# Optimization experiments

Hardware: AMD Instinct MI355X
Metric: run time of the kernel (lower is better)

## Reference

```python
import jax, jax.numpy as jnp
import numpy as np
from math import factorial

LAMBDA_MAX = 3
NU_MAX = 4
B = 200000

# --- Clebsch-Gordan coefficients (Racah formula), precomputed on host ---

def _cg_np(l1, l2, L):
    f = factorial
    C = np.zeros((2 * l1 + 1, 2 * l2 + 1, 2 * L + 1), dtype=np.float64)
    pref0 = np.sqrt((2 * L + 1) * f(L + l1 - l2) * f(L - l1 + l2) * f(l1 + l2 - L) / f(l1 + l2 + L + 1))
    for m1 in range(-l1, l1 + 1):
        for m2 in range(-l2, l2 + 1):
            M = m1 + m2
            if abs(M) > L:
                continue
            pref = pref0 * np.sqrt(f(L + M) * f(L - M) * f(l1 - m1) * f(l1 + m1) * f(l2 - m2) * f(l2 + m2))
            s = 0.0
            for k in range(0, l1 + l2 - L + 1):
                if l1 - m1 - k < 0 or l2 + m2 - k < 0 or L - l2 + m1 + k < 0 or L - l1 - m2 + k < 0:
                    continue
                s += (-1) ** k / (f(k) * f(l1 + l2 - L - k) * f(l1 - m1 - k) * f(l2 + m2 - k) * f(L - l2 + m1 + k) * f(L - l1 - m2 + k))
            C[m1 + l1, m2 + l2, M + L] = pref * s
    return C

_CG = {}

def cg(l1, l2, L):
    key = (l1, l2, L)
    if key not in _CG:
        _CG[key] = jnp.asarray(_cg_np(l1, l2, L), dtype=jnp.float32)
    return _CG[key]

# --- WignerCombiningUnrolled: CG tensor product of two equivariant kernel dicts ---

def combine(X1, X2, lam_max):
    out = {}
    for k1, K1 in X1.items():
        l1, s1 = (int(t) for t in k1.split('_'))
        for k2, K2 in X2.items():
            l2, s2 = (int(t) for t in k2.split('_'))
            for L in range(abs(l1 - l2), min(l1 + l2, lam_max) + 1):
                sig = s1 * s2 * (-1) ** (l1 + l2 + L)
                C = cg(l1, l2, L)  # [2l1+1, 2l2+1, 2L+1]
                # K_out[b,mu,mu'] = C[m1,m2,mu] C[m1',m2',mu'] K1[b,m1,m1'] K2[b,m2,m2']
                contrib = jnp.einsum('mnk,pqj,bmp,bnq->bkj', C, C, K1, K2, optimize=True)
                key = str(L) + '_' + str(sig)
                out[key] = out[key] + contrib if key in out else contrib
    return out


def setup_inputs() -> dict:
    key = jax.random.key(0)
    ks = jax.random.split(key, 4)
    return {
        'x0': jax.random.normal(ks[0], (B, 1, 1), dtype=jnp.float32),
        'x1': jax.random.normal(ks[1], (B, 3, 3), dtype=jnp.float32),
        'x2': jax.random.normal(ks[2], (B, 5, 5), dtype=jnp.float32),
        'x3': jax.random.normal(ks[3], (B, 7, 7), dtype=jnp.float32),
    }


def reference(x0, x1, x2, x3):
    # nu=1 kernels: keys 'l_1' for l = 0..lambda_max
    X = {str(l) + '_1': x for l, x in enumerate([x0, x1, x2, x3])}
    equivariant_kernels = [X]
    result = [X['0_1'][:, 0, 0, None]]
    for nu in range(2, NU_MAX + 1):
        if nu <= NU_MAX - NU_MAX // 2:
            equivariant_kernels.append(combine(equivariant_kernels[-1], equivariant_kernels[0], LAMBDA_MAX))
            result.append(equivariant_kernels[-1]['0_1'][:, 0, 0, None])
        else:
            comb = combine(
                equivariant_kernels[NU_MAX - NU_MAX // 2 - 1],
                equivariant_kernels[nu - NU_MAX + NU_MAX // 2 - 1],
                0,
            )
            result.append(comb['0_1'][:, 0, 0, None])
    return jnp.concatenate(result, axis=-1)  # [B, nu_max]
```

## Files before the change

kernel.cpp:

```cpp
#include <hip/hip_runtime.h>


#define SCHED_FENCE() __builtin_amdgcn_sched_barrier(0)

template <int N>
__device__ __forceinline__ void opaque(float (&A)[N]) {
#pragma unroll
  for (int i = 0; i < N; ++i) asm volatile("" : "+v"(A[i]));
}
__device__ __forceinline__ void opaque1(float& x) { asm volatile("" : "+v"(x)); }

constexpr double cfact(int n) { double r = 1.0; for (int i = 2; i <= n; ++i) r *= (double)i; return r; }

constexpr double csqrt(double x) {
  if (x <= 0.0) return 0.0;
  double g = x > 1.0 ? x : 1.0;
  for (int i = 0; i < 100; ++i) g = 0.5 * (g + x / g);
  return g;
}

constexpr double cg_val(int l1, int l2, int L, int m1, int m2) {
  const int M = m1 + m2;
  if (M < -L || M > L) return 0.0;
  const double pref0 = csqrt((2.0 * L + 1.0) * cfact(L + l1 - l2) * cfact(L - l1 + l2) *
                             cfact(l1 + l2 - L) / cfact(l1 + l2 + L + 1));
  const double pref = pref0 * csqrt(cfact(L + M) * cfact(L - M) * cfact(l1 - m1) *
                                    cfact(l1 + m1) * cfact(l2 - m2) * cfact(l2 + m2));
  double s = 0.0;
  for (int k = 0; k <= l1 + l2 - L; ++k) {
    if (l1 - m1 - k < 0 || l2 + m2 - k < 0 || L - l2 + m1 + k < 0 || L - l1 - m2 + k < 0) continue;
    const double t = 1.0 / (cfact(k) * cfact(l1 + l2 - L - k) * cfact(l1 - m1 - k) *
                            cfact(l2 + m2 - k) * cfact(L - l2 + m1 + k) * cfact(L - l1 - m2 + k));
    s += (k & 1) ? -t : t;
  }
  return pref * s;
}

template <int l1, int l2, int L>
struct CG2T {
  double a[2 * l1 + 1][2 * L + 1];
  constexpr CG2T() : a{} {
    for (int mi = 0; mi < 2 * l1 + 1; ++mi)
      for (int kk = 0; kk < 2 * L + 1; ++kk) {
        const int m1 = mi - l1, M = kk - L, m2 = M - m1;
        a[mi][kk] = (m2 < -l2 || m2 > l2) ? 0.0 : cg_val(l1, l2, L, m1, m2);
      }
  }
};
template <int l1, int l2, int L>
constexpr CG2T<l1, l2, L> CG2v = CG2T<l1, l2, L>();

template <int l1, int l2, int L, int W>
__device__ __forceinline__ float triElem(const float (&K1)[(2 * l1 + 1) * (2 * l1 + 1)],
                                         const float (&K2)[(2 * l2 + 1) * (2 * l2 + 1)],
                                         int kk, int jj) {
  constexpr int d1 = 2 * l1 + 1, d2 = 2 * l2 + 1;
  float a0 = 0.f, a1 = 0.f;
#pragma unroll
  for (int mi = 0; mi < d1; ++mi) {
    const int ni = (kk - L) - (mi - l1) + l2;
    if (ni < 0 || ni >= d2) continue;
#pragma unroll
    for (int pi = 0; pi < d1; ++pi) {
      const int qi = (jj - L) - (pi - l1) + l2;
      if (qi < 0 || qi >= d2) continue;
      const double c0 = CG2v<l1, l2, L>.a[mi][kk] * CG2v<l1, l2, L>.a[pi][jj];
      if (c0 == 0.0) continue;
      double c = c0 * (double)W;
      if constexpr (l1 == l2) {
        const int id1 = mi * d1 + pi, id2 = ni * d1 + qi;
        if (id1 > id2) continue;
        if (id1 < id2) c *= 2.0;
      }
      if ((mi + pi) & 1)
        a1 = fmaf((float)c * K1[mi * d1 + pi], K2[ni * d2 + qi], a1);
      else
        a0 = fmaf((float)c * K1[mi * d1 + pi], K2[ni * d2 + qi], a0);
    }
  }
  return a0 + a1;
}

template <int l, bool HAS_O3, typename F>
__device__ __forceinline__ void reduceKey(F yel, const float (&Xl)[(2 * l + 1) * (2 * l + 1)],
                                          float& o3, float& o4) {
  constexpr int d = 2 * l + 1;
  constexpr float inv = 1.0f / (float)d;
#pragma unroll
  for (int i = 0; i < d; ++i) {
#pragma unroll
    for (int j = 0; j < d; ++j) {
      const int id = i * d + j, id2 = d * d - 1 - id;
      if (id > id2) continue;
      const float c = (((i + j) & 1) ? -inv : inv);
      const float y1 = yel(i, j);
      if (id == id2) {
        o4 = fmaf(c * y1, y1, o4);
        if constexpr (HAS_O3) o3 = fmaf(c * y1, Xl[id2], o3);
      } else {
        const float y2 = yel(2 * l - i, 2 * l - j);
        o4 = fmaf((2.0f * c) * y1, y2, o4);
        if constexpr (HAS_O3) {
          o3 = fmaf(c * y1, Xl[id2], o3);
          o3 = fmaf(c * y2, Xl[id], o3);
        }
      }
    }
  }
}

__global__ __launch_bounds__(256)
__attribute__((amdgpu_waves_per_eu(2, 2)))
void wigner_kernel(
    const float* __restrict__ x0, const float* __restrict__ x1,
    const float* __restrict__ x2, const float* __restrict__ x3,
    float* __restrict__ out, int n) {
  const int b = blockIdx.x * blockDim.x + threadIdx.x;
  if (b >= n) return;

  float X0[1], X1[9], X2[25], X3[49];
  X0[0] = x0[b];
#pragma unroll
  for (int i = 0; i < 9; ++i) X1[i] = x1[b * 9 + i];
#pragma unroll
  for (int i = 0; i < 25; ++i) X2[i] = x2[b * 25 + i];
#pragma unroll
  for (int i = 0; i < 49; ++i) X3[i] = x3[b * 49 + i];

  float o2, o3 = 0.f, o4 = 0.f;

#define KEY_FENCE()                                                   \
  do {                                                                \
    opaque(X0); opaque(X1); opaque(X2); opaque(X3);                   \
    opaque1(o3); opaque1(o4);                                         \
    SCHED_FENCE();                                                    \
  } while (0)

  KEY_FENCE();

  {
    float y = triElem<0, 0, 0, 1>(X0, X0, 0, 0)
            + triElem<1, 1, 0, 1>(X1, X1, 0, 0)
            + triElem<2, 2, 0, 1>(X2, X2, 0, 0)
            + triElem<3, 3, 0, 1>(X3, X3, 0, 0);
    o2 = y;
    o3 = fmaf(y, X0[0], o3);
    o4 = fmaf(y, y, o4);
  }
  KEY_FENCE();
  {
    auto yel = [&](int i, int j) {
      return triElem<0, 1, 1, 2>(X0, X1, i, j)
           + triElem<1, 2, 1, 2>(X1, X2, i, j)
           + triElem<2, 3, 1, 2>(X2, X3, i, j);
    };
    reduceKey<1, true>(yel, X1, o3, o4);
  }
  KEY_FENCE();
  {
    auto yel = [&](int i, int j) {
      return triElem<1, 1, 1, 1>(X1, X1, i, j)
           + triElem<2, 2, 1, 1>(X2, X2, i, j)
           + triElem<3, 3, 1, 1>(X3, X3, i, j);
    };
    reduceKey<1, false>(yel, X1, o3, o4);
  }
  KEY_FENCE();
  {
    auto yel = [&](int i, int j) {
      return triElem<0, 2, 2, 2>(X0, X2, i, j)
           + triElem<1, 1, 2, 1>(X1, X1, i, j)
           + triElem<1, 3, 2, 2>(X1, X3, i, j)
           + triElem<2, 2, 2, 1>(X2, X2, i, j)
           + triElem<3, 3, 2, 1>(X3, X3, i, j);
    };
    reduceKey<2, true>(yel, X2, o3, o4);
  }
  KEY_FENCE();
  {
    auto yel = [&](int i, int j) {
      return triElem<1, 2, 2, 2>(X1, X2, i, j)
           + triElem<2, 3, 2, 2>(X2, X3, i, j);
    };
    reduceKey<2, false>(yel, X2, o3, o4);
  }
  KEY_FENCE();
  {
    auto yel = [&](int i, int j) {
      return triElem<0, 3, 3, 2>(X0, X3, i, j)
           + triElem<1, 2, 3, 2>(X1, X2, i, j)
           + triElem<2, 3, 3, 2>(X2, X3, i, j);
    };
    reduceKey<3, true>(yel, X3, o3, o4);
  }
  KEY_FENCE();
  {
    auto yel = [&](int i, int j) {
      return triElem<1, 3, 3, 2>(X1, X3, i, j)
           + triElem<2, 2, 3, 1>(X2, X2, i, j)
           + triElem<3, 3, 3, 1>(X3, X3, i, j);
    };
    reduceKey<3, false>(yel, X3, o3, o4);
  }
#undef KEY_FENCE

  reinterpret_cast<float4*>(out)[b] = make_float4(X0[0], o2, o3, o4);
}

extern "C" void kernel_launch(void* const* d_in, const int* in_sizes, int n_in,
                              void* d_out, int out_size, void* d_ws, size_t ws_size,
                              hipStream_t stream) {
  const float* x0 = (const float*)d_in[0];
  const float* x1 = (const float*)d_in[1];
  const float* x2 = (const float*)d_in[2];
  const float* x3 = (const float*)d_in[3];
  float* out = (float*)d_out;
  const int n = in_sizes[0];
  const int block = 256;
  const int grid = (n + block - 1) / block;
  wigner_kernel<<<grid, block, 0, stream>>>(x0, x1, x2, x3, out, n);
}
```

Measured before the change: 126.6 us.

## Process two batch elements per thread with packed float2 FMA

Each thread now handles two batch elements, b and b+half, held in float2 vectors, so the arithmetic can map to packed FP32 FMA instructions (v_pk_fma_f32) that do two lanes per instruction. Block size drops to 64 and the grid is halved to match. The goal is to raise FP32 throughput in this compute-bound contraction. In exchange, register pressure roughly doubles and may cause spills, and the two input streams are loaded at strided offsets.

```diff
diff --git a/kernel.cpp b/kernel.cpp
--- a/kernel.cpp
+++ b/kernel.cpp
@@ -1,14 +1,20 @@
 #include <hip/hip_runtime.h>
 
 
+typedef float v2f __attribute__((ext_vector_type(2)));
+
 #define SCHED_FENCE() __builtin_amdgcn_sched_barrier(0)
 
 template <int N>
-__device__ __forceinline__ void opaque(float (&A)[N]) {
+__device__ __forceinline__ void opaque(v2f (&A)[N]) {
 #pragma unroll
   for (int i = 0; i < N; ++i) asm volatile("" : "+v"(A[i]));
 }
-__device__ __forceinline__ void opaque1(float& x) { asm volatile("" : "+v"(x)); }
+__device__ __forceinline__ void opaque1(v2f& x) { asm volatile("" : "+v"(x)); }
+
+__device__ __forceinline__ v2f vfma(v2f a, v2f b, v2f c) {
+  return __builtin_elementwise_fma(a, b, c);
+}
 
 constexpr double cfact(int n) { double r = 1.0; for (int i = 2; i <= n; ++i) r *= (double)i; return r; }
 
@@ -51,11 +57,11 @@
 constexpr CG2T<l1, l2, L> CG2v = CG2T<l1, l2, L>();
 
 template <int l1, int l2, int L, int W>
-__device__ __forceinline__ float triElem(const float (&K1)[(2 * l1 + 1) * (2 * l1 + 1)],
-                                         const float (&K2)[(2 * l2 + 1) * (2 * l2 + 1)],
-                                         int kk, int jj) {
+__device__ __forceinline__ v2f triElem(const v2f (&K1)[(2 * l1 + 1) * (2 * l1 + 1)],
+                                       const v2f (&K2)[(2 * l2 + 1) * (2 * l2 + 1)],
+                                       int kk, int jj) {
   constexpr int d1 = 2 * l1 + 1, d2 = 2 * l2 + 1;
-  float a0 = 0.f, a1 = 0.f;
+  v2f a0 = {0.f, 0.f}, a1 = {0.f, 0.f};
 #pragma unroll
   for (int mi = 0; mi < d1; ++mi) {
     const int ni = (kk - L) - (mi - l1) + l2;
@@ -73,17 +79,17 @@
         if (id1 < id2) c *= 2.0;
       }
       if ((mi + pi) & 1)
-        a1 = fmaf((float)c * K1[mi * d1 + pi], K2[ni * d2 + qi], a1);
+        a1 = vfma((float)c * K1[mi * d1 + pi], K2[ni * d2 + qi], a1);
       else
-        a0 = fmaf((float)c * K1[mi * d1 + pi], K2[ni * d2 + qi], a0);
+        a0 = vfma((float)c * K1[mi * d1 + pi], K2[ni * d2 + qi], a0);
     }
   }
   return a0 + a1;
 }
 
 template <int l, bool HAS_O3, typename F>
-__device__ __forceinline__ void reduceKey(F yel, const float (&Xl)[(2 * l + 1) * (2 * l + 1)],
-                                          float& o3, float& o4) {
+__device__ __forceinline__ void reduceKey(F yel, const v2f (&Xl)[(2 * l + 1) * (2 * l + 1)],
+                                          v2f& o3, v2f& o4) {
   constexpr int d = 2 * l + 1;
   constexpr float inv = 1.0f / (float)d;
 #pragma unroll
@@ -93,41 +99,46 @@
       const int id = i * d + j, id2 = d * d - 1 - id;
       if (id > id2) continue;
       const float c = (((i + j) & 1) ? -inv : inv);
-      const float y1 = yel(i, j);
+      const v2f y1 = yel(i, j);
       if (id == id2) {
-        o4 = fmaf(c * y1, y1, o4);
-        if constexpr (HAS_O3) o3 = fmaf(c * y1, Xl[id2], o3);
+        o4 = vfma(c * y1, y1, o4);
+        if constexpr (HAS_O3) o3 = vfma(c * y1, Xl[id2], o3);
       } else {
-        const float y2 = yel(2 * l - i, 2 * l - j);
-        o4 = fmaf((2.0f * c) * y1, y2, o4);
+        const v2f y2 = yel(2 * l - i, 2 * l - j);
+        o4 = vfma((2.0f * c) * y1, y2, o4);
         if constexpr (HAS_O3) {
-          o3 = fmaf(c * y1, Xl[id2], o3);
-          o3 = fmaf(c * y2, Xl[id], o3);
+          o3 = vfma(c * y1, Xl[id2], o3);
+          o3 = vfma(c * y2, Xl[id], o3);
         }
       }
     }
   }
 }
 
-__global__ __launch_bounds__(256)
+__global__ __launch_bounds__(64)
 __attribute__((amdgpu_waves_per_eu(2, 2)))
 void wigner_kernel(
     const float* __restrict__ x0, const float* __restrict__ x1,
     const float* __restrict__ x2, const float* __restrict__ x3,
     float* __restrict__ out, int n) {
-  const int b = blockIdx.x * blockDim.x + threadIdx.x;
-  if (b >= n) return;
-
-  float X0[1], X1[9], X2[25], X3[49];
-  X0[0] = x0[b];
-#pragma unroll
-  for (int i = 0; i < 9; ++i) X1[i] = x1[b * 9 + i];
-#pragma unroll
-  for (int i = 0; i < 25; ++i) X2[i] = x2[b * 25 + i];
-#pragma unroll
-  for (int i = 0; i < 49; ++i) X3[i] = x3[b * 49 + i];
-
-  float o2, o3 = 0.f, o4 = 0.f;
+  const int half = (n + 1) / 2;
+  const int t = blockIdx.x * blockDim.x + threadIdx.x;
+  if (t >= half) return;
+  const int b0 = t;
+  const int b1 = t + half;
+  const bool two = (b1 < n);
+  const int b1c = two ? b1 : b0;
+
+  v2f X0[1], X1[9], X2[25], X3[49];
+  X0[0] = (v2f){x0[b0], x0[b1c]};
+#pragma unroll
+  for (int i = 0; i < 9; ++i) X1[i] = (v2f){x1[b0 * 9 + i], x1[b1c * 9 + i]};
+#pragma unroll
+  for (int i = 0; i < 25; ++i) X2[i] = (v2f){x2[b0 * 25 + i], x2[b1c * 25 + i]};
+#pragma unroll
+  for (int i = 0; i < 49; ++i) X3[i] = (v2f){x3[b0 * 49 + i], x3[b1c * 49 + i]};
+
+  v2f o2 = {0.f, 0.f}, o3 = {0.f, 0.f}, o4 = {0.f, 0.f};
 
 #define KEY_FENCE()                                                   \
   do {                                                                \
@@ -139,13 +150,13 @@
   KEY_FENCE();
 
   {
-    float y = triElem<0, 0, 0, 1>(X0, X0, 0, 0)
-            + triElem<1, 1, 0, 1>(X1, X1, 0, 0)
-            + triElem<2, 2, 0, 1>(X2, X2, 0, 0)
-            + triElem<3, 3, 0, 1>(X3, X3, 0, 0);
+    v2f y = triElem<0, 0, 0, 1>(X0, X0, 0, 0)
+          + triElem<1, 1, 0, 1>(X1, X1, 0, 0)
+          + triElem<2, 2, 0, 1>(X2, X2, 0, 0)
+          + triElem<3, 3, 0, 1>(X3, X3, 0, 0);
     o2 = y;
-    o3 = fmaf(y, X0[0], o3);
-    o4 = fmaf(y, y, o4);
+    o3 = vfma(y, X0[0], o3);
+    o4 = vfma(y, y, o4);
   }
   KEY_FENCE();
   {
@@ -204,7 +215,9 @@
   }
 #undef KEY_FENCE
 
-  reinterpret_cast<float4*>(out)[b] = make_float4(X0[0], o2, o3, o4);
+  float4* out4 = reinterpret_cast<float4*>(out);
+  out4[b0] = make_float4(X0[0].x, o2.x, o3.x, o4.x);
+  if (two) out4[b1] = make_float4(X0[0].y, o2.y, o3.y, o4.y);
 }
 
 extern "C" void kernel_launch(void* const* d_in, const int* in_sizes, int n_in,
@@ -216,7 +229,8 @@
   const float* x3 = (const float*)d_in[3];
   float* out = (float*)d_out;
   const int n = in_sizes[0];
-  const int block = 256;
-  const int grid = (n + block - 1) / block;
+  const int half = (n + 1) / 2;
+  const int block = 64;
+  const int grid = (half + block - 1) / block;
   wigner_kernel<<<grid, block, 0, stream>>>(x0, x1, x2, x3, out, n);
 }
```

New measurement: 293.8 us. 2.32x slower.
